# Kernel tuning notes

Measured on AMD Instinct MI355X. Metric: run time of the kernel, lower is better.

The kernel has to match this reference:

```python
import jax, jax.numpy as jnp
import numpy as np

P = 200_000   # pedestrians
T = 16        # frames in targets/outputs
F_DIR = 15    # tracklet_length - 5 frames used by direction loss


def _conv_bbox(b):
    # Faithful to the source's in-place convert_bbox, which (due to sequential
    # in-place updates) maps [a,b,c,d] -> [a-c/2, b-d/2, a, b].
    a, bb, c, d = b[..., 0], b[..., 1], b[..., 2], b[..., 3]
    return jnp.stack([a - 0.5 * c, bb - 0.5 * d, a, bb], axis=-1)


def _corner_pts(b):
    # 5 reference points: center, lt(x0,y0), rt(x0,y1), lb(x1,y0), rb(x1,y1)
    x0, y0, x1, y1 = b[..., 0], b[..., 1], b[..., 2], b[..., 3]
    xs = jnp.stack([0.5 * (x0 + x1), x0, x0, x1, x1], axis=-1)
    ys = jnp.stack([0.5 * (y0 + y1), y0, y1, y0, y1], axis=-1)
    return xs, ys


def _unit_dir(fx, fy, tx, ty):
    dy, dx = ty - fy, tx - fx
    n = jnp.sqrt(dy * dy + dx * dx) + 1e-6
    return dy / n, dx / n


def _direction_loss(outputs, targets):
    last = targets[:F_DIR, :, :4]
    pred = last + outputs[:F_DIR]
    true = targets[1:F_DIR + 1, :, :4]
    # Source mutates `targets` in place: frames 1..14 get convert_bbox applied
    # TWICE when reused as `last_abs` (once as prior frame's true_abs). Replicate.
    last_c1 = _conv_bbox(last)
    last_eff = jnp.concatenate([last_c1[:1], _conv_bbox(last_c1[1:])], axis=0)
    pred_c = _conv_bbox(pred)
    true_c = _conv_bbox(true)
    lx, ly = _corner_pts(last_eff)   # [F_DIR, P, 5]
    px, py = _corner_pts(pred_c)
    tx, ty = _corner_pts(true_c)
    pdy, pdx = _unit_dir(lx, ly, px, py)
    tdy, tdx = _unit_dir(lx, ly, tx, ty)
    cosang = jnp.clip(pdy * tdy + pdx * tdx, -1.0, 1.0)
    weight = 0.2
    return weight * jnp.sum(jnp.arccos(cosang)) / (targets.shape[1] * F_DIR)


def setup_inputs() -> dict:
    key = jax.random.key(0)
    k1, k2 = jax.random.split(key)
    outputs = jax.random.normal(k1, (T, P, 4), dtype=jnp.float32) * 0.1
    targets = jax.random.uniform(k2, (T, P, 8), dtype=jnp.float32)
    return {"outputs": outputs, "targets": targets}


def reference(outputs, targets):
    delta = targets[:, :, 4:8]
    d = outputs - delta
    ad = jnp.abs(d)
    sl1 = jnp.where(ad < 1.0, 0.5 * d * d, ad - 0.5)  # smooth_l1, beta=1
    loss_o = jnp.sum(sl1, axis=2) / targets.shape[1]   # [T, P]
    loss_dir = _direction_loss(outputs, targets)
    return 0.99 * loss_o + 0.01 * loss_dir
```

## Files before the change

### kernel.cpp

```cpp
#include <hip/hip_runtime.h>

#define BS 256

__device__ __forceinline__ float fast_acos(float x) {
    float ax = fabsf(x);
    float s  = sqrtf(fmaxf(0.f, 1.f - ax));
    float p  = fmaf(ax, fmaf(ax, fmaf(ax, -0.0187293f, 0.0742610f), -0.2121144f), 1.5707288f);
    float r  = s * p;
    return (x >= 0.f) ? r : 3.14159265358979f - r;
}

__device__ __forceinline__ float dir_item(float4 L, float4 O, float4 Tn, bool first) {
    float pa = L.x + O.x, pb = L.y + O.y, pc = L.z + O.z, pd = L.w + O.w;
    float Px0 = pa - 0.5f * pc, Py0 = pb - 0.5f * pd, Px1 = pa, Py1 = pb;
    float Tx0 = Tn.x - 0.5f * Tn.z, Ty0 = Tn.y - 0.5f * Tn.w, Tx1 = Tn.x, Ty1 = Tn.y;
    float Lx1 = L.x - 0.5f * L.z, Ly1 = L.y - 0.5f * L.w;
    float Lx0, Ly0;
    if (first) { Lx0 = Lx1; Ly0 = Ly1; Lx1 = L.x; Ly1 = L.y; }
    else       { Lx0 = 0.5f * (L.x - L.z); Ly0 = 0.5f * (L.y - L.w); }

    float lxs[5] = {0.5f * (Lx0 + Lx1), Lx0, Lx0, Lx1, Lx1};
    float lys[5] = {0.5f * (Ly0 + Ly1), Ly0, Ly1, Ly0, Ly1};
    float pxs[5] = {0.5f * (Px0 + Px1), Px0, Px0, Px1, Px1};
    float pys[5] = {0.5f * (Py0 + Py1), Py0, Py1, Py0, Py1};
    float txs[5] = {0.5f * (Tx0 + Tx1), Tx0, Tx0, Tx1, Tx1};
    float tys[5] = {0.5f * (Ty0 + Ty1), Ty0, Ty1, Ty0, Ty1};

    float acc = 0.f;
    #pragma unroll
    for (int k = 0; k < 5; ++k) {
        float pdx = pxs[k] - lxs[k], pdy = pys[k] - lys[k];
        float tdx = txs[k] - lxs[k], tdy = tys[k] - lys[k];
        float p2  = pdx * pdx + pdy * pdy;
        float t2  = tdx * tdx + tdy * tdy;
        float dot = pdx * tdx + pdy * tdy;
        float inv = rsqrtf(p2 * t2);
        float cosang = fminf(1.0f, fmaxf(-1.0f, dot * inv));
        acc += fast_acos(cosang);
    }
    return acc;
}

__device__ __forceinline__ float sl1_4(float4 O, float4 D) {
    float s = 0.f;
    { float d = O.x - D.x, ad = fabsf(d); s += (ad < 1.f) ? 0.5f * d * d : ad - 0.5f; }
    { float d = O.y - D.y, ad = fabsf(d); s += (ad < 1.f) ? 0.5f * d * d : ad - 0.5f; }
    { float d = O.z - D.z, ad = fabsf(d); s += (ad < 1.f) ? 0.5f * d * d : ad - 0.5f; }
    { float d = O.w - D.w, ad = fabsf(d); s += (ad < 1.f) ? 0.5f * d * d : ad - 0.5f; }
    return s;
}

#define LD4(ptr) (*reinterpret_cast<const float4*>(ptr))

__global__ __launch_bounds__(BS, 4) __attribute__((amdgpu_waves_per_eu(4, 4)))
void fused_kernel(const float* __restrict__ outputs,
                  const float* __restrict__ targets,
                  float* __restrict__ out,
                  float* __restrict__ partials,
                  int P, float w) {
    __shared__ float smem[BS / 64];
    long long gid = (long long)blockIdx.x * BS + threadIdx.x;
    float acc = 0.f;
    if (gid < 4ll * P) {
        int grp     = (int)(gid / P);
        long long p = gid - (long long)grp * P;
        const long long ts8 = 8ll * P, os4 = 4ll * P;
        const float* tb = targets + ((long long)(grp * 4) * P + p) * 8;
        const float* ob = outputs + ((long long)(grp * 4) * P + p) * 4;
        float*       wb = out + (long long)(grp * 4) * P + p;
        const bool has4 = (grp < 3);

        float4 Tf0 = LD4(tb);
        float4 Tf1 = LD4(tb + ts8);
        float4 Tf2 = LD4(tb + 2 * ts8);
        float4 Tf3 = LD4(tb + 3 * ts8);
        float4 Ts0 = LD4(tb + 4);
        float4 Ts1 = LD4(tb + ts8 + 4);
        float4 Ts2 = LD4(tb + 2 * ts8 + 4);
        float4 Ts3 = LD4(tb + 3 * ts8 + 4);
        float4 O0  = LD4(ob);
        float4 O1  = LD4(ob + os4);
        float4 O2  = LD4(ob + 2 * os4);
        float4 O3  = LD4(ob + 3 * os4);
        float4 Tf4 = has4 ? LD4(tb + 4 * ts8) : make_float4(0.f, 0.f, 0.f, 0.f);

        asm volatile("" ::
            "v"(Tf0.x), "v"(Tf1.x), "v"(Tf2.x), "v"(Tf3.x), "v"(Tf4.x),
            "v"(Ts0.x), "v"(Ts1.x), "v"(Ts2.x), "v"(Ts3.x),
            "v"(O0.x),  "v"(O1.x),  "v"(O2.x),  "v"(O3.x));

        wb[0]       = sl1_4(O0, Ts0) * w;
        wb[P]       = sl1_4(O1, Ts1) * w;
        wb[2ll * P] = sl1_4(O2, Ts2) * w;
        wb[3ll * P] = sl1_4(O3, Ts3) * w;

        acc  = dir_item(Tf0, O0, Tf1, grp == 0);
        acc += dir_item(Tf1, O1, Tf2, false);
        acc += dir_item(Tf2, O2, Tf3, false);
        if (has4) acc += dir_item(Tf3, O3, Tf4, false);
    }
    #pragma unroll
    for (int off = 32; off > 0; off >>= 1) acc += __shfl_down(acc, off, 64);
    int lane = threadIdx.x & 63, w64 = threadIdx.x >> 6;
    if (lane == 0) smem[w64] = acc;
    __syncthreads();
    if (threadIdx.x == 0) {
        float r = 0.f;
        #pragma unroll
        for (int i = 0; i < BS / 64; ++i) r += smem[i];
        partials[blockIdx.x] = r;
    }
}

__global__ void finalize_kernel(const float* __restrict__ partials, int nb,
                                float* __restrict__ out, long long n4, int P) {
    __shared__ double dsm[BS / 64];
    __shared__ float c_sh;
    double dacc = 0.0;
    for (int i = threadIdx.x; i < nb; i += BS) dacc += (double)partials[i];
    #pragma unroll
    for (int off = 32; off > 0; off >>= 1) dacc += __shfl_down(dacc, off, 64);
    int lane = threadIdx.x & 63, w = threadIdx.x >> 6;
    if (lane == 0) dsm[w] = dacc;
    __syncthreads();
    if (threadIdx.x == 0) {
        double tot = dsm[0] + dsm[1] + dsm[2] + dsm[3];
        c_sh = (float)(0.01 * 0.2 * tot / ((double)P * 15.0));
    }
    __syncthreads();
    float c = c_sh;

    float4* o4 = reinterpret_cast<float4*>(out);
    long long stride = (long long)gridDim.x * blockDim.x;
    for (long long i = (long long)blockIdx.x * blockDim.x + threadIdx.x; i < n4; i += stride) {
        float4 v = o4[i];
        v.x += c; v.y += c; v.z += c; v.w += c;
        o4[i] = v;
    }
}

extern "C" void kernel_launch(void* const* d_in, const int* in_sizes, int n_in,
                              void* d_out, int out_size, void* d_ws, size_t ws_size,
                              hipStream_t stream) {
    const float* outputs = (const float*)d_in[0];
    const float* targets = (const float*)d_in[1];
    float* out = (float*)d_out;
    float* partials = (float*)d_ws;

    const int T = 16;
    int P = in_sizes[0] / (T * 4);

    long long nthreads = 4ll * P;
    int nb1 = (int)((nthreads + BS - 1) / BS);
    fused_kernel<<<nb1, BS, 0, stream>>>(outputs, targets, out, partials,
                                         P, 0.99f / (float)P);

    long long n4 = (long long)out_size / 4;
    int nb2 = (int)((n4 + BS - 1) / BS);
    if (nb2 > 2048) nb2 = 2048;
    finalize_kernel<<<nb2, BS, 0, stream>>>(partials, nb1, out, n4, P);
}
```

Before: 45.14 us.

## Pack direction math into float2 vectors, relax occupancy hints, rework finalize grid

```diff
diff --git a/kernel.cpp b/kernel.cpp
--- a/kernel.cpp
+++ b/kernel.cpp
@@ -1,6 +1,8 @@
 #include <hip/hip_runtime.h>
 
 #define BS 256
+
+typedef float f32x2 __attribute__((ext_vector_type(2)));
 
 __device__ __forceinline__ float fast_acos(float x) {
     float ax = fabsf(x);
@@ -11,29 +13,33 @@
 }
 
 __device__ __forceinline__ float dir_item(float4 L, float4 O, float4 Tn, bool first) {
-    float pa = L.x + O.x, pb = L.y + O.y, pc = L.z + O.z, pd = L.w + O.w;
-    float Px0 = pa - 0.5f * pc, Py0 = pb - 0.5f * pd, Px1 = pa, Py1 = pb;
-    float Tx0 = Tn.x - 0.5f * Tn.z, Ty0 = Tn.y - 0.5f * Tn.w, Tx1 = Tn.x, Ty1 = Tn.y;
-    float Lx1 = L.x - 0.5f * L.z, Ly1 = L.y - 0.5f * L.w;
-    float Lx0, Ly0;
-    if (first) { Lx0 = Lx1; Ly0 = Ly1; Lx1 = L.x; Ly1 = L.y; }
-    else       { Lx0 = 0.5f * (L.x - L.z); Ly0 = 0.5f * (L.y - L.w); }
+    f32x2 LA = {L.x, L.y},  LB = {L.z, L.w};
+    f32x2 OA = {O.x, O.y},  OB = {O.z, O.w};
+    f32x2 TA = {Tn.x, Tn.y}, TB = {Tn.z, Tn.w};
 
-    float lxs[5] = {0.5f * (Lx0 + Lx1), Lx0, Lx0, Lx1, Lx1};
-    float lys[5] = {0.5f * (Ly0 + Ly1), Ly0, Ly1, Ly0, Ly1};
-    float pxs[5] = {0.5f * (Px0 + Px1), Px0, Px0, Px1, Px1};
-    float pys[5] = {0.5f * (Py0 + Py1), Py0, Py1, Py0, Py1};
-    float txs[5] = {0.5f * (Tx0 + Tx1), Tx0, Tx0, Tx1, Tx1};
-    float tys[5] = {0.5f * (Ty0 + Ty1), Ty0, Ty1, Ty0, Ty1};
+    f32x2 PA = LA + OA, PB = LB + OB;
+    f32x2 P0 = PA - 0.5f * PB, P1 = PA;
+    f32x2 T0 = TA - 0.5f * TB, T1 = TA;
+    f32x2 Lc1 = LA - 0.5f * LB;
+    f32x2 L0, L1;
+    if (first) { L0 = Lc1; L1 = LA; }
+    else       { L0 = 0.5f * (LA - LB); L1 = Lc1; }
+
+    f32x2 l[5] = {0.5f * (L0 + L1), L0, {L0.x, L1.y}, {L1.x, L0.y}, L1};
+    f32x2 p[5] = {0.5f * (P0 + P1), P0, {P0.x, P1.y}, {P1.x, P0.y}, P1};
+    f32x2 t[5] = {0.5f * (T0 + T1), T0, {T0.x, T1.y}, {T1.x, T0.y}, T1};
 
     float acc = 0.f;
     #pragma unroll
     for (int k = 0; k < 5; ++k) {
-        float pdx = pxs[k] - lxs[k], pdy = pys[k] - lys[k];
-        float tdx = txs[k] - lxs[k], tdy = tys[k] - lys[k];
-        float p2  = pdx * pdx + pdy * pdy;
-        float t2  = tdx * tdx + tdy * tdy;
-        float dot = pdx * tdx + pdy * tdy;
+        f32x2 dp = p[k] - l[k];
+        f32x2 dt = t[k] - l[k];
+        f32x2 sp = dp * dp;
+        f32x2 st = dt * dt;
+        f32x2 dv = dp * dt;
+        float p2  = sp.x + sp.y;
+        float t2  = st.x + st.y;
+        float dot = dv.x + dv.y;
         float inv = rsqrtf(p2 * t2);
         float cosang = fminf(1.0f, fmaxf(-1.0f, dot * inv));
         acc += fast_acos(cosang);
@@ -52,7 +58,7 @@
 
 #define LD4(ptr) (*reinterpret_cast<const float4*>(ptr))
 
-__global__ __launch_bounds__(BS, 4) __attribute__((amdgpu_waves_per_eu(4, 4)))
+__global__ __launch_bounds__(BS)
 void fused_kernel(const float* __restrict__ outputs,
                   const float* __restrict__ targets,
                   float* __restrict__ out,
@@ -84,11 +90,6 @@
         float4 O3  = LD4(ob + 3 * os4);
         float4 Tf4 = has4 ? LD4(tb + 4 * ts8) : make_float4(0.f, 0.f, 0.f, 0.f);
 
-        asm volatile("" ::
-            "v"(Tf0.x), "v"(Tf1.x), "v"(Tf2.x), "v"(Tf3.x), "v"(Tf4.x),
-            "v"(Ts0.x), "v"(Ts1.x), "v"(Ts2.x), "v"(Ts3.x),
-            "v"(O0.x),  "v"(O1.x),  "v"(O2.x),  "v"(O3.x));
-
         wb[0]       = sl1_4(O0, Ts0) * w;
         wb[P]       = sl1_4(O1, Ts1) * w;
         wb[2ll * P] = sl1_4(O2, Ts2) * w;
@@ -112,16 +113,17 @@
     }
 }
 
-__global__ void finalize_kernel(const float* __restrict__ partials, int nb,
-                                float* __restrict__ out, long long n4, int P) {
+__global__ __launch_bounds__(BS)
+void finalize_kernel(const float* __restrict__ partials, int nb,
+                     float* __restrict__ out, int P) {
     __shared__ double dsm[BS / 64];
     __shared__ float c_sh;
     double dacc = 0.0;
     for (int i = threadIdx.x; i < nb; i += BS) dacc += (double)partials[i];
     #pragma unroll
     for (int off = 32; off > 0; off >>= 1) dacc += __shfl_down(dacc, off, 64);
-    int lane = threadIdx.x & 63, w = threadIdx.x >> 6;
-    if (lane == 0) dsm[w] = dacc;
+    int lane = threadIdx.x & 63, wv = threadIdx.x >> 6;
+    if (lane == 0) dsm[wv] = dacc;
     __syncthreads();
     if (threadIdx.x == 0) {
         double tot = dsm[0] + dsm[1] + dsm[2] + dsm[3];
@@ -130,12 +132,15 @@
     __syncthreads();
     float c = c_sh;
 
-    float4* o4 = reinterpret_cast<float4*>(out);
-    long long stride = (long long)gridDim.x * blockDim.x;
-    for (long long i = (long long)blockIdx.x * blockDim.x + threadIdx.x; i < n4; i += stride) {
-        float4 v = o4[i];
-        v.x += c; v.y += c; v.z += c; v.w += c;
-        o4[i] = v;
+    long long gid = (long long)blockIdx.x * BS + threadIdx.x;
+    if (gid < 4ll * P) {
+        int grp     = (int)(gid / P);
+        long long p = gid - (long long)grp * P;
+        float* wb = out + (long long)(grp * 4) * P + p;
+        wb[0]       += c;
+        wb[P]       += c;
+        wb[2ll * P] += c;
+        wb[3ll * P] += c;
     }
 }
 
@@ -150,13 +155,10 @@
     const int T = 16;
     int P = in_sizes[0] / (T * 4);
 
-    long long nthreads = 4ll * P;
-    int nb1 = (int)((nthreads + BS - 1) / BS);
+    long long units = 4ll * P;
+    int nb1 = (int)((units + BS - 1) / BS);
+
     fused_kernel<<<nb1, BS, 0, stream>>>(outputs, targets, out, partials,
                                          P, 0.99f / (float)P);
-
-    long long n4 = (long long)out_size / 4;
-    int nb2 = (int)((n4 + BS - 1) / BS);
-    if (nb2 > 2048) nb2 = 2048;
-    finalize_kernel<<<nb2, BS, 0, stream>>>(partials, nb1, out, n4, P);
+    finalize_kernel<<<nb1, BS, 0, stream>>>(partials, nb1, out, P);
 }
```

Result: slower. 49.05 us (+8.7%).
